# Performance work log

Hardware: AMD Instinct MI355X
Metric: run time of the kernel (lower is better)

Reference implementation:

```python
import jax, jax.numpy as jnp
import numpy as np

TOKENS, DIM, DIM_OUT, R, ALPHA = 8192, 4096, 4096, 16, 32
SCALE = ALPHA / R  # 2.0


def setup_inputs() -> dict:
    key = jax.random.key(0)
    k1, k2, k3, k4, k5 = jax.random.split(key, 5)
    x = jax.random.normal(k1, (TOKENS, DIM), dtype=jnp.float32)
    A = jax.random.normal(k2, (DIM, R), dtype=jnp.float32)
    B = jax.random.normal(k3, (R, DIM_OUT), dtype=jnp.float32) * 0.02
    W = jax.random.normal(k4, (DIM_OUT, DIM), dtype=jnp.float32) * 0.02  # base Linear weight
    b = jax.random.normal(k5, (DIM_OUT,), dtype=jnp.float32)
    return {"x": x, "A": A, "B": B, "W": W, "b": b}


def reference(x, A, B, W, b):
    # LoRA path: x @ (A @ B) * scale, computed in the efficient low-rank order
    # (mathematically identical to materializing the full-rank weight).
    lora = ((x @ A) @ B) * SCALE              # [tokens, dim_out]
    base = x @ W.T + b                         # wrapped base Linear forward
    return lora + base
```

## Files before the change

kernel.cpp:

```cpp
#include <hip/hip_runtime.h>
#include <hip/hip_bf16.h>
#include <stdint.h>

#define TOKENS   8192
#define DIM      4096
#define DIM_OUT  4096
#define LORA_R   16
#define LORA_SCALE 2.0f

typedef __bf16 bf16_t;
typedef __attribute__((ext_vector_type(8))) __bf16 bfrag;
typedef __attribute__((ext_vector_type(4))) float f32x4;

__device__ __forceinline__ void gload_lds16(const bf16_t* gsrc, bf16_t* ldst) {
    __builtin_amdgcn_global_load_lds(
        (const __attribute__((address_space(1))) uint32_t*)(const void*)gsrc,
        (__attribute__((address_space(3))) uint32_t*)(void*)ldst,
        16, 0, 0);
}

__global__ void cast_x_kernel(const float* __restrict__ x, bf16_t* __restrict__ xb) {
    const int total = TOKENS * DIM / 8;
    for (int i = blockIdx.x * blockDim.x + threadIdx.x; i < total;
         i += gridDim.x * blockDim.x) {
        const float4* p = reinterpret_cast<const float4*>(x + (size_t)i * 8);
        float4 v0 = p[0], v1 = p[1];
        union { bf16_t o[8]; uint4 u; } pk;
        pk.o[0] = (bf16_t)v0.x; pk.o[1] = (bf16_t)v0.y;
        pk.o[2] = (bf16_t)v0.z; pk.o[3] = (bf16_t)v0.w;
        pk.o[4] = (bf16_t)v1.x; pk.o[5] = (bf16_t)v1.y;
        pk.o[6] = (bf16_t)v1.z; pk.o[7] = (bf16_t)v1.w;
        *reinterpret_cast<uint4*>(xb + (size_t)i * 8) = pk.u;
    }
}

__global__ void weff_kernel(const float* __restrict__ W, const float* __restrict__ A,
                            const float* __restrict__ B, bf16_t* __restrict__ Wt) {
    int idx = blockIdx.x * blockDim.x + threadIdx.x;
    int k0 = (idx & 511) << 3;
    int n0 = (idx >> 9) << 2;

    float bn[4][16];
#pragma unroll
    for (int r = 0; r < 16; ++r) {
        float4 bv = *reinterpret_cast<const float4*>(B + (size_t)r * DIM_OUT + n0);
        bn[0][r] = bv.x; bn[1][r] = bv.y; bn[2][r] = bv.z; bn[3][r] = bv.w;
    }
    float ab[4][8];
#pragma unroll
    for (int j = 0; j < 8; ++j) {
        const float4* ap = reinterpret_cast<const float4*>(A + (size_t)(k0 + j) * LORA_R);
        float4 a0 = ap[0], a1 = ap[1], a2 = ap[2], a3 = ap[3];
        float av[16] = {a0.x,a0.y,a0.z,a0.w,a1.x,a1.y,a1.z,a1.w,
                        a2.x,a2.y,a2.z,a2.w,a3.x,a3.y,a3.z,a3.w};
#pragma unroll
        for (int n = 0; n < 4; ++n) {
            float s = 0.f;
#pragma unroll
            for (int r = 0; r < 16; ++r) s += av[r] * bn[n][r];
            ab[n][j] = s;
        }
    }
#pragma unroll
    for (int n = 0; n < 4; ++n) {
        const float4* wp = reinterpret_cast<const float4*>(W + (size_t)(n0 + n) * DIM + k0);
        float4 w0 = wp[0], w1 = wp[1];
        float wv[8] = {w0.x,w0.y,w0.z,w0.w,w1.x,w1.y,w1.z,w1.w};
        union { bf16_t o[8]; uint4 u; } pk;
#pragma unroll
        for (int j = 0; j < 8; ++j) pk.o[j] = (bf16_t)(wv[j] + LORA_SCALE * ab[n][j]);
        *reinterpret_cast<uint4*>(Wt + (size_t)(n0 + n) * DIM + k0) = pk.u;
    }
}

#define BM 256
#define BN 256
#define BK 64
#define MB_BLKS (TOKENS / BM)
#define NB_BLKS (DIM_OUT / BN)
#define NT      (DIM / BK)
#define ITERS   (NT / 2)

#define BAR() do { __builtin_amdgcn_s_barrier(); __builtin_amdgcn_sched_barrier(0); } while (0)
#define VMWAIT_(n) asm volatile("s_waitcnt vmcnt(" #n ")" ::: "memory")
#define VMWAIT(n) VMWAIT_(n)

__global__ __launch_bounds__(512, 2) void gemm_kernel(
    const bf16_t* __restrict__ Xb, const bf16_t* __restrict__ Wt,
    const float* __restrict__ bias, float* __restrict__ C)
{
    __shared__ __align__(16) bf16_t sA[2][BM][BK];
    __shared__ __align__(16) bf16_t sB[2][BN][BK];

    const int nwg = MB_BLKS * NB_BLKS;
    int bid = blockIdx.x;
    int swz = (bid & 7) * (nwg >> 3) + (bid >> 3);
    int bm = swz / NB_BLKS;
    int bn = swz % NB_BLKS;

    const int tid  = threadIdx.x;
    const int lane = tid & 63;
    const int wid  = tid >> 6;
    const int wr   = wid >> 2;
    const int wc   = wid & 3;

    const int srow = tid >> 3;
    const int scol = (tid & 7) * 8;
    const int koff = (((tid & 7) ^ ((tid >> 3) & 7)) * 8);
    const bf16_t* Ag = Xb + (size_t)(bm * BM + srow) * DIM + koff;
    const bf16_t* Bg = Wt + (size_t)(bn * BN + srow) * DIM + koff;

#define STAGE_A(d, kt) do { \
    const bf16_t* s_ = Ag + (size_t)(kt) * BK; \
    bf16_t* d_ = &sA[d][srow][scol]; \
    gload_lds16(s_,                     d_); \
    gload_lds16(s_ + (size_t)64  * DIM, d_ + 64  * BK); \
    gload_lds16(s_ + (size_t)128 * DIM, d_ + 128 * BK); \
    gload_lds16(s_ + (size_t)192 * DIM, d_ + 192 * BK); \
} while (0)

#define STAGE_B(d, kt) do { \
    const bf16_t* s_ = Bg + (size_t)(kt) * BK; \
    bf16_t* d_ = &sB[d][srow][scol]; \
    gload_lds16(s_,                     d_); \
    gload_lds16(s_ + (size_t)64  * DIM, d_ + 64  * BK); \
    gload_lds16(s_ + (size_t)128 * DIM, d_ + 128 * BK); \
    gload_lds16(s_ + (size_t)192 * DIM, d_ + 192 * BK); \
} while (0)

    const int q     = lane & 7;
    const int kslot = lane >> 4;
    const int r15   = lane & 15;
    const int cK0   = ((kslot    ) ^ q) * 8;
    const int cK1   = ((kslot + 4) ^ q) * 8;
    const int arow0 = wr * 128 + r15;
    const int brow0 = wc * 64  + r15;

    f32x4 acc[8][4] = {};
    bfrag af[4][2], bf[4][2];

#define LOAD_A(d, mb) do { \
    _Pragma("unroll") \
    for (int m_ = 0; m_ < 4; ++m_) { \
        af[m_][0] = *reinterpret_cast<const bfrag*>(&sA[d][arow0 + (mb + m_) * 16][cK0]); \
        af[m_][1] = *reinterpret_cast<const bfrag*>(&sA[d][arow0 + (mb + m_) * 16][cK1]); \
    } \
} while (0)

#define LOAD_B2(d, nb) do { \
    _Pragma("unroll") \
    for (int n_ = 0; n_ < 2; ++n_) { \
        bf[nb + n_][0] = *reinterpret_cast<const bfrag*>(&sB[d][brow0 + (nb + n_) * 16][cK0]); \
        bf[nb + n_][1] = *reinterpret_cast<const bfrag*>(&sB[d][brow0 + (nb + n_) * 16][cK1]); \
    } \
} while (0)

#define MFMA_Q(mb, nb) do { \
    __builtin_amdgcn_s_setprio(1); \
    _Pragma("unroll") \
    for (int m_ = 0; m_ < 4; ++m_) \
    _Pragma("unroll") \
    for (int n_ = 0; n_ < 2; ++n_) \
    _Pragma("unroll") \
    for (int ks_ = 0; ks_ < 2; ++ks_) \
        acc[mb + m_][nb + n_] = __builtin_amdgcn_mfma_f32_16x16x32_bf16( \
            af[m_][ks_], bf[nb + n_][ks_], acc[mb + m_][nb + n_], 0, 0, 0); \
    __builtin_amdgcn_s_setprio(0); \
} while (0)

#define TILE_PHASES(d, ktn, DO_STAGE, VM) do { \
     LOAD_A(d, 0); LOAD_B2(d, 0); BAR(); MFMA_Q(0, 0); BAR(); \
     LOAD_B2(d, 2);               BAR(); MFMA_Q(0, 2); BAR(); \
     LOAD_A(d, 4); if (DO_STAGE) STAGE_B(d, ktn); \
                                          BAR(); MFMA_Q(4, 0); BAR(); \
     if (DO_STAGE) STAGE_A(d, ktn); \
                                          BAR(); MFMA_Q(4, 2); \
             VMWAIT(VM); BAR(); \
} while (0)

    STAGE_A(0, 0); STAGE_B(0, 0);
    STAGE_A(1, 1); STAGE_B(1, 1);
    VMWAIT(8);
    BAR();

    for (int it = 0; it < ITERS - 1; ++it) {
        int kt0 = 2 * it;
        TILE_PHASES(0, kt0 + 2, true, 8);
        TILE_PHASES(1, kt0 + 3, true, 8);
    }
    TILE_PHASES(0, 0, false, 0);
    TILE_PHASES(1, 0, false, 0);

    int row0 = bm * BM + wr * 128 + (lane >> 4) * 4;
    int col0 = bn * BN + wc * 64 + r15;
#pragma unroll
    for (int n = 0; n < 4; ++n) {
        int c = col0 + n * 16;
        float bv = bias[c];
#pragma unroll
        for (int m = 0; m < 8; ++m) {
            int r = row0 + m * 16;
#pragma unroll
            for (int j = 0; j < 4; ++j)
                C[(size_t)(r + j) * DIM_OUT + c] = acc[m][n][j] + bv;
        }
    }
}

extern "C" void kernel_launch(void* const* d_in, const int* in_sizes, int n_in,
                              void* d_out, int out_size, void* d_ws, size_t ws_size,
                              hipStream_t stream) {
    const float* x = (const float*)d_in[0];
    const float* A = (const float*)d_in[1];
    const float* B = (const float*)d_in[2];
    const float* W = (const float*)d_in[3];
    const float* b = (const float*)d_in[4];
    float* out = (float*)d_out;

    bf16_t* xb = (bf16_t*)d_ws;
    bf16_t* Wt = (bf16_t*)((char*)d_ws + (size_t)TOKENS * DIM * 2);

    cast_x_kernel<<<2048, 256, 0, stream>>>(x, xb);
    weff_kernel<<<(DIM_OUT * DIM / 32) / 256, 256, 0, stream>>>(W, A, B, Wt);
    gemm_kernel<<<MB_BLKS * NB_BLKS, 512, 0, stream>>>(xb, Wt, b, out);
}
```

Baseline: 340.3 us.

## Double-buffer LDS fragment registers and prefetch next tile's fragments across phases

```diff
diff --git a/kernel.cpp b/kernel.cpp
--- a/kernel.cpp
+++ b/kernel.cpp
@@ -79,9 +79,9 @@
 #define MB_BLKS (TOKENS / BM)
 #define NB_BLKS (DIM_OUT / BN)
 #define NT      (DIM / BK)
-#define ITERS   (NT / 2)
 
 #define BAR() do { __builtin_amdgcn_s_barrier(); __builtin_amdgcn_sched_barrier(0); } while (0)
+#define SB0() __builtin_amdgcn_sched_barrier(0)
 #define VMWAIT_(n) asm volatile("s_waitcnt vmcnt(" #n ")" ::: "memory")
 #define VMWAIT(n) VMWAIT_(n)
 
@@ -137,25 +137,25 @@
     const int brow0 = wc * 64  + r15;
 
     f32x4 acc[8][4] = {};
-    bfrag af[4][2], bf[4][2];
-
-#define LOAD_A(d, mb) do { \
+    bfrag aLo[4][2], aHi[4][2], bLo[2][2], bHi[2][2];
+
+#define READ_A4(dst, dd, mb) do { \
     _Pragma("unroll") \
     for (int m_ = 0; m_ < 4; ++m_) { \
-        af[m_][0] = *reinterpret_cast<const bfrag*>(&sA[d][arow0 + (mb + m_) * 16][cK0]); \
-        af[m_][1] = *reinterpret_cast<const bfrag*>(&sA[d][arow0 + (mb + m_) * 16][cK1]); \
+        dst[m_][0] = *reinterpret_cast<const bfrag*>(&sA[dd][arow0 + (mb + m_) * 16][cK0]); \
+        dst[m_][1] = *reinterpret_cast<const bfrag*>(&sA[dd][arow0 + (mb + m_) * 16][cK1]); \
     } \
 } while (0)
 
-#define LOAD_B2(d, nb) do { \
+#define READ_B2(dst, dd, nb) do { \
     _Pragma("unroll") \
     for (int n_ = 0; n_ < 2; ++n_) { \
-        bf[nb + n_][0] = *reinterpret_cast<const bfrag*>(&sB[d][brow0 + (nb + n_) * 16][cK0]); \
-        bf[nb + n_][1] = *reinterpret_cast<const bfrag*>(&sB[d][brow0 + (nb + n_) * 16][cK1]); \
+        dst[n_][0] = *reinterpret_cast<const bfrag*>(&sB[dd][brow0 + (nb + n_) * 16][cK0]); \
+        dst[n_][1] = *reinterpret_cast<const bfrag*>(&sB[dd][brow0 + (nb + n_) * 16][cK1]); \
     } \
 } while (0)
 
-#define MFMA_Q(mb, nb) do { \
+#define MFMA_Q(Af, Bf, mb, nb) do { \
     __builtin_amdgcn_s_setprio(1); \
     _Pragma("unroll") \
     for (int m_ = 0; m_ < 4; ++m_) \
@@ -164,32 +164,34 @@
     _Pragma("unroll") \
     for (int ks_ = 0; ks_ < 2; ++ks_) \
         acc[mb + m_][nb + n_] = __builtin_amdgcn_mfma_f32_16x16x32_bf16( \
-            af[m_][ks_], bf[nb + n_][ks_], acc[mb + m_][nb + n_], 0, 0, 0); \
+            Af[m_][ks_], Bf[n_][ks_], acc[mb + m_][nb + n_], 0, 0, 0); \
     __builtin_amdgcn_s_setprio(0); \
 } while (0)
 
-#define TILE_PHASES(d, ktn, DO_STAGE, VM) do { \
-     LOAD_A(d, 0); LOAD_B2(d, 0); BAR(); MFMA_Q(0, 0); BAR(); \
-     LOAD_B2(d, 2);               BAR(); MFMA_Q(0, 2); BAR(); \
-     LOAD_A(d, 4); if (DO_STAGE) STAGE_B(d, ktn); \
-                                          BAR(); MFMA_Q(4, 0); BAR(); \
-     if (DO_STAGE) STAGE_A(d, ktn); \
-                                          BAR(); MFMA_Q(4, 2); \
-             VMWAIT(VM); BAR(); \
+#define TILE(d, ktn, DO_STAGE, DO_NEXT, VM) do { \
+     READ_B2(bHi, d, 2); \
+             SB0(); MFMA_Q(aLo, bLo, 0, 0); BAR(); \
+     READ_A4(aHi, d, 4); if (DO_STAGE) STAGE_B(d, ktn); \
+             SB0(); MFMA_Q(aLo, bHi, 0, 2); VMWAIT(VM); BAR(); \
+     if (DO_NEXT) READ_A4(aLo, (d) ^ 1, 0); if (DO_STAGE) STAGE_A(d, ktn); \
+             SB0(); MFMA_Q(aHi, bHi, 4, 2); BAR(); \
+     MFMA_Q(aHi, bLo, 4, 0); \
+             if (DO_NEXT) READ_B2(bLo, (d) ^ 1, 0); BAR(); \
 } while (0)
 
     STAGE_A(0, 0); STAGE_B(0, 0);
-    STAGE_A(1, 1); STAGE_B(1, 1);
+    STAGE_B(1, 1); STAGE_A(1, 1);
     VMWAIT(8);
     BAR();
-
-    for (int it = 0; it < ITERS - 1; ++it) {
+    READ_A4(aLo, 0, 0); READ_B2(bLo, 0, 0);
+
+    for (int it = 0; it < NT / 2 - 1; ++it) {
         int kt0 = 2 * it;
-        TILE_PHASES(0, kt0 + 2, true, 8);
-        TILE_PHASES(1, kt0 + 3, true, 8);
-    }
-    TILE_PHASES(0, 0, false, 0);
-    TILE_PHASES(1, 0, false, 0);
+        TILE(0, kt0 + 2, true, true, 4);
+        TILE(1, kt0 + 3, true, true, 4);
+    }
+    TILE(0, 0, false, true, 0);
+    TILE(1, 0, false, false, 0);
 
     int row0 = bm * BM + wr * 128 + (lane >> 4) * 4;
     int col0 = bn * BN + wc * 64 + r15;
```

New measurement: 329.4 us. 1.03x faster.
